# Optimization experiments

Measured on AMD Instinct MI355X. Metric: run time of the kernel, lower is better.

Reference implementation:

```python
import jax, jax.numpy as jnp
import numpy as np

# ---- module configuration (from init_kwargs) ----
NX, NV = 2048, 1024
LX = 1.0
VMAX = 6.0
DX = LX / NX
DV = 2.0 * VMAX / NV
XS = jnp.linspace(-LX / 2 + DX / 2, LX / 2 - DX / 2, NX)
VS = jnp.linspace(-VMAX + DV / 2, VMAX - DV / 2, NV)
AE, AI = 1.0, 1836.0
ZE, ZI = -1.0, 1.0
OMEGA_C_TAU = 1.0
NU_EE, NU_II = 1.0, 0.1
DT = 1e-3
T_LBO = 1.0  # LBO temperature, u = 0


def minmod(a, b):
    return jnp.where(a * b > 0, jnp.sign(a) * jnp.minimum(jnp.abs(a), jnp.abs(b)), 0.0)


def _sl(a, lo, hi, axis):
    return jax.lax.slice_in_dim(a, lo, hi, axis=axis)


def slope_limited_flux_divergence(f_pad, F, dx, axis):
    # f_pad has N+4 cells along `axis` (2 ghost cells per side). MUSCL + minmod.
    n = f_pad.shape[axis]
    d = _sl(f_pad, 1, n, axis) - _sl(f_pad, 0, n - 1, axis)          # n-1 diffs
    sigma = minmod(_sl(d, 0, n - 2, axis), _sl(d, 1, n - 1, axis))    # slopes for cells 1..n-2
    fc = _sl(f_pad, 1, n - 1, axis)                                   # cells 1..n-2
    m = n - 2
    fL = _sl(fc, 0, m - 1, axis) + 0.5 * _sl(sigma, 0, m - 1, axis)   # left interface states
    fR = _sl(fc, 1, m, axis) - 0.5 * _sl(sigma, 1, m, axis)           # right interface states
    flux = F(fL, fR)                                                  # N+1 interface fluxes
    k = flux.shape[axis]
    return (_sl(flux, 1, k, axis) - _sl(flux, 0, k - 1, axis)) / dx   # N cells


def pad_x_periodic(f):
    return jnp.concatenate([f[-2:, :], f, f[:2, :]], axis=0)


def pad_v_zero(f):
    z = jnp.zeros((f.shape[0], 2), f.dtype)
    return jnp.concatenate([z, f, z], axis=1)


def poisson_solve(rho_c):
    # dE/dx = rho_c, zero-mean E (periodic-compatible gauge)
    E = jnp.cumsum(rho_c) * DX
    return E - jnp.mean(E)


def species_rhs(f, E, A, Z):
    v = VS[None, :]
    Fx = lambda l, r: jnp.where(v > 0, l * v, r * v)                  # upwind in x
    vdfdx = slope_limited_flux_divergence(pad_x_periodic(f), Fx, DX, axis=0)
    Ec = (OMEGA_C_TAU * Z / A) * E[:, None]
    Fv = lambda l, r: jnp.where(Ec > 0, l * Ec, r * Ec)               # upwind in v
    Edfdv = slope_limited_flux_divergence(pad_v_zero(f), Fv, DV, axis=1)
    return -vdfdx - Edfdv


def vlasov_rhs(fe, fi):
    ne = jnp.sum(fe, axis=1) * DV
    ni = jnp.sum(fi, axis=1) * DV
    E = poisson_solve(ZE * ne + ZI * ni)
    return species_rhs(fe, E, AE, ZE), species_rhs(fi, E, AI, ZI)


def ssprk2(fe, fi, dt):
    re, ri = vlasov_rhs(fe, fi)
    fe1, fi1 = fe + dt * re, fi + dt * ri
    re1, ri1 = vlasov_rhs(fe1, fi1)
    return 0.5 * (fe + fe1 + dt * re1), 0.5 * (fi + fi1 + dt * ri1)


def lbo_diagonals(lam):
    # L f = lam * d/dv( v f + T df/dv ), central differences
    vm = jnp.roll(VS, 1)
    vp = jnp.roll(VS, -1)
    dl = lam * (T_LBO / DV**2 - vm / (2 * DV))
    du = lam * (T_LBO / DV**2 + vp / (2 * DV))
    d = lam * (-2.0 * T_LBO / DV**2) * jnp.ones(NV, XS.dtype)
    return dl.at[0].set(0.0), d, du.at[-1].set(0.0)


def nu_shape():
    midpt = LX / 3
    ef = LX / 6 / 10
    h0 = lambda x: 1 + jnp.exp(x / ef - midpt / ef)
    return 1.0 / (0.5 * (h0(XS) + h0(-XS)))  # [Nx]


def thomas(dl, d, du, b):
    # Thomas algorithm; dl[0]==0 and du[-1]==0 assumed.
    def fwd(carry, inp):
        cp, bp = carry
        dli, di, dui, bi = inp
        m = di - dli * cp
        cpi = dui / m
        bpi = (bi - dli * bp) / m
        return (cpi, bpi), (cpi, bpi)
    z = jnp.zeros((), b.dtype)
    _, (cp, bp) = jax.lax.scan(fwd, (z, z), (dl, d, du, b))
    def bwd(x_next, inp):
        cpi, bpi = inp
        x = bpi - cpi * x_next
        return x, x
    _, x = jax.lax.scan(bwd, z, (cp, bp), reverse=True)
    return x


def implicit_collide(f, lam, dt):
    dl, d, du = lbo_diagonals(lam)
    nu = nu_shape()
    def solve_row(nui, frow):
        return thomas(-dt * nui * dl, 1.0 - dt * nui * d, -dt * nui * du, frow)
    return jax.vmap(solve_row)(nu, f)


def setup_inputs() -> dict:
    key = jax.random.key(0)
    k1, k2 = jax.random.split(key)
    fe = jax.random.uniform(k1, (NX, NV), dtype=jnp.float32)
    fi = jax.random.uniform(k2, (NX, NV), dtype=jnp.float32)
    return {"fe": fe, "fi": fi}


def reference(fe, fi):
    fe1, fi1 = ssprk2(fe, fi, DT)
    fe2 = implicit_collide(fe1, NU_EE, DT)
    fi2 = implicit_collide(fi1, NU_II, DT)
    return jnp.stack([fe2, fi2])  # [2, Nx, Nv]
```

## Files before the change

### kernel.cpp

```cpp
#include <hip/hip_runtime.h>
#include <math.h>

#define NX 2048
#define NV 1024
static constexpr float DXf   = 1.0f / 2048.0f;
static constexpr float DVf   = 12.0f / 1024.0f;
static constexpr float DTf   = 0.001f;
static constexpr float INV_DX = 2048.0f;
static constexpr float INV_DV = 1024.0f / 12.0f;

__device__ __forceinline__ float minmod_f(float a, float b) {
    return (a * b > 0.0f) ? (a > 0.0f ? fminf(a, b) : fmaxf(a, b)) : 0.0f;
}

__device__ __forceinline__ float frcp(float x) {
    float r = __builtin_amdgcn_rcpf(x);
    return r * (2.0f - x * r);
}

__device__ __forceinline__ void rhs4(const float* __restrict__ g, int i, int j0, float Ec,
                                     float4& f0v, float4& rv) {
    const float* rowc = g + i * NV;
    const float* rm1  = g + (((i - 1) & (NX - 1)) * NV);
    const float* rm2  = g + (((i - 2) & (NX - 1)) * NV);
    const float* rp1  = g + (((i + 1) & (NX - 1)) * NV);
    const float* rp2  = g + (((i + 2) & (NX - 1)) * NV);

    float4 c   = *(const float4*)(rowc + j0);
    float4 xm1 = *(const float4*)(rm1 + j0);
    float4 xm2 = *(const float4*)(rm2 + j0);
    float4 xp1 = *(const float4*)(rp1 + j0);
    float4 xp2 = *(const float4*)(rp2 + j0);
    float4 lm = make_float4(0.f, 0.f, 0.f, 0.f);
    float4 rp = make_float4(0.f, 0.f, 0.f, 0.f);
    if (j0 >= 4)      lm = *(const float4*)(rowc + j0 - 4);
    if (j0 <= NV - 8) rp = *(const float4*)(rowc + j0 + 4);

    float vals[8] = {lm.z, lm.w, c.x, c.y, c.z, c.w, rp.x, rp.y};
    const float* cc   = (const float*)&c;
    const float* am1  = (const float*)&xm1;
    const float* am2  = (const float*)&xm2;
    const float* ap1  = (const float*)&xp1;
    const float* ap2  = (const float*)&xp2;
    float* f0o = (float*)&f0v;
    float* ro  = (float*)&rv;

    #pragma unroll
    for (int k = 0; k < 4; ++k) {
        float f0  = cc[k];
        float fm1 = am1[k], fm2 = am2[k], fp1 = ap1[k], fp2 = ap2[k];

        float v = DVf * ((float)(j0 + k) + 0.5f) - 6.0f;
        float dm1 = fm1 - fm2, d0 = f0 - fm1, dp1 = fp1 - f0, dp2 = fp2 - fp1;
        float sm1 = minmod_f(dm1, d0);
        float s0  = minmod_f(d0, dp1);
        float sp1 = minmod_f(dp1, dp2);
        float PhiM, PhiP;
        if (v > 0.0f) {
            PhiM = (fm1 + 0.5f * sm1) * v;
            PhiP = (f0  + 0.5f * s0 ) * v;
        } else {
            PhiM = (f0  - 0.5f * s0 ) * v;
            PhiP = (fp1 - 0.5f * sp1) * v;
        }
        float vdfdx = (PhiP - PhiM) * INV_DX;

        float gm2 = vals[k], gm1 = vals[k + 1], gp1 = vals[k + 3], gp2 = vals[k + 4];
        float em1 = gm1 - gm2, e0 = f0 - gm1, ep1 = gp1 - f0, ep2 = gp2 - gp1;
        float tm1 = minmod_f(em1, e0);
        float t0  = minmod_f(e0, ep1);
        float tp1 = minmod_f(ep1, ep2);
        float GM, GP;
        if (Ec > 0.0f) {
            GM = (gm1 + 0.5f * tm1) * Ec;
            GP = (f0  + 0.5f * t0 ) * Ec;
        } else {
            GM = (f0  - 0.5f * t0 ) * Ec;
            GP = (gp1 - 0.5f * tp1) * Ec;
        }
        float Edfdv = (GP - GM) * INV_DV;

        f0o[k] = f0;
        ro[k]  = -vdfdx - Edfdv;
    }
}

__device__ __forceinline__ float compute_E(const float* __restrict__ se,
                                           const float* __restrict__ si, int i) {
    int t = threadIdx.x;
    float pref = 0.0f, wtot = 0.0f;
    #pragma unroll
    for (int q = 0; q < NX / 256; ++q) {
        int k = q * 256 + t;
        float rho = DVf * (si[k] - se[k]);
        if (k <= i) pref += rho;
        wtot += rho * (float)(NX - k);
    }
    #pragma unroll
    for (int off = 32; off > 0; off >>= 1) {
        pref += __shfl_down(pref, off, 64);
        wtot += __shfl_down(wtot, off, 64);
    }
    __shared__ float sp[4], sw[4];
    int lane = t & 63, wave = t >> 6;
    if (lane == 0) { sp[wave] = pref; sw[wave] = wtot; }
    __syncthreads();
    float P = sp[0] + sp[1] + sp[2] + sp[3];
    float W = sw[0] + sw[1] + sw[2] + sw[3];
    return DXf * (P - W * (1.0f / (float)NX));
}

__global__ __launch_bounds__(256) void moments_kernel(const float* __restrict__ fe,
                                                      const float* __restrict__ fi,
                                                      float* __restrict__ se,
                                                      float* __restrict__ si) {
    int i = blockIdx.x;
    int t = threadIdx.x;
    float4 a4 = *(const float4*)(fe + (size_t)i * NV + 4 * t);
    float4 b4 = *(const float4*)(fi + (size_t)i * NV + 4 * t);
    float a = a4.x + a4.y + a4.z + a4.w;
    float b = b4.x + b4.y + b4.z + b4.w;
    __shared__ float r1[4], r2[4];
    #pragma unroll
    for (int off = 32; off > 0; off >>= 1) {
        a += __shfl_down(a, off, 64);
        b += __shfl_down(b, off, 64);
    }
    int lane = t & 63, wave = t >> 6;
    if (lane == 0) { r1[wave] = a; r2[wave] = b; }
    __syncthreads();
    if (t == 0) {
        se[i] = r1[0] + r1[1] + r1[2] + r1[3];
        si[i] = r2[0] + r2[1] + r2[2] + r2[3];
    }
}

__global__ __launch_bounds__(256) void stage1_kernel(const float* __restrict__ fe,
                                                     const float* __restrict__ fi,
                                                     const float* __restrict__ se,
                                                     const float* __restrict__ si,
                                                     float* __restrict__ fe1,
                                                     float* __restrict__ fi1,
                                                     float* __restrict__ se1,
                                                     float* __restrict__ si1) {
    int i  = blockIdx.x;
    int sp = blockIdx.y;
    const float* g = sp ? fi : fe;
    float* out = sp ? fi1 : fe1;
    float zoa = sp ? (1.0f / 1836.0f) : -1.0f;
    float Ec = zoa * compute_E(se, si, i);
    int t = threadIdx.x;
    int j0 = 4 * t;

    float4 f0v, rv;
    rhs4(g, i, j0, Ec, f0v, rv);
    float4 o;
    o.x = f0v.x + DTf * rv.x;
    o.y = f0v.y + DTf * rv.y;
    o.z = f0v.z + DTf * rv.z;
    o.w = f0v.w + DTf * rv.w;
    *(float4*)(out + i * NV + j0) = o;

    float x = o.x + o.y + o.z + o.w;
    #pragma unroll
    for (int off = 32; off > 0; off >>= 1) x += __shfl_down(x, off, 64);
    __shared__ float sred[4];
    int lane = t & 63, wave = t >> 6;
    if (lane == 0) sred[wave] = x;
    __syncthreads();
    if (t == 0) { (sp ? si1 : se1)[i] = sred[0] + sred[1] + sred[2] + sred[3]; }
}

__global__ __launch_bounds__(256) void stage2_collide_kernel(const float* __restrict__ fe,
                                                             const float* __restrict__ fi,
                                                             const float* __restrict__ fe1,
                                                             const float* __restrict__ fi1,
                                                             const float* __restrict__ se1,
                                                             const float* __restrict__ si1,
                                                             float* __restrict__ out) {
    const float Tdv2   = 1.0f / (DVf * DVf);
    const float inv2dv = 0.5f / DVf;

    int i  = blockIdx.x;
    int sp = blockIdx.y;
    const float* h = sp ? fi : fe;
    const float* g = sp ? fi1 : fe1;
    float* orow = out + ((size_t)sp * NX + i) * NV;
    float zoa = sp ? (1.0f / 1836.0f) : -1.0f;
    float lam = sp ? 0.1f : 1.0f;
    float Ec = zoa * compute_E(se1, si1, i);
    int t = threadIdx.x;
    int lane = t & 63;
    int wave = t >> 6;

    __shared__ float lds_f[NV + NV / 16];

    {
        int j0 = 4 * t;
        float4 f0v, rv;
        rhs4(g, i, j0, Ec, f0v, rv);
        float4 h4 = *(const float4*)(h + i * NV + j0);
        int a = j0 + (j0 >> 4);
        lds_f[a]     = 0.5f * h4.x + 0.5f * f0v.x + (0.5f * DTf) * rv.x;
        lds_f[a + 1] = 0.5f * h4.y + 0.5f * f0v.y + (0.5f * DTf) * rv.y;
        lds_f[a + 2] = 0.5f * h4.z + 0.5f * f0v.z + (0.5f * DTf) * rv.z;
        lds_f[a + 3] = 0.5f * h4.w + 0.5f * f0v.w + (0.5f * DTf) * rv.w;
    }
    __syncthreads();
    if (wave != 0) return;

    float xi = DXf * ((float)i + 0.5f) - 0.5f;
    float nu = 1.0f / (1.0f + 0.5f * (expf(60.0f * xi - 20.0f) + expf(-60.0f * xi - 20.0f)));
    float K = DTf * nu * lam;
    float b = 1.0f + 2.0f * K * Tdv2;

    float Dv[16], Av[16], Cv[16];
    int j0 = lane * 16;
    int base = 17 * lane;
    #pragma unroll
    for (int r = 0; r < 16; ++r) {
        int j = j0 + r;
        float d = lds_f[base + r];
        float a = (j == 0)      ? 0.0f : -K * (Tdv2 - (DVf * ((float)j - 0.5f) - 6.0f) * inv2dv);
        float c = (j == NV - 1) ? 0.0f : -K * (Tdv2 + (DVf * ((float)j + 1.5f) - 6.0f) * inv2dv);
        if (r == 0) {
            float e = frcp(b);
            Dv[0] = e * d;
            Av[0] = e * a;
            Cv[0] = e * c;
        } else {
            float e = frcp(b - a * Cv[r - 1]);
            Dv[r] = e * (d - a * Dv[r - 1]);
            Av[r] = -e * a * Av[r - 1];
            Cv[r] = e * c;
        }
    }
    #pragma unroll
    for (int r = 14; r >= 0; --r) {
        Dv[r] = Dv[r] - Cv[r] * Dv[r + 1];
        Av[r] = Av[r] - Cv[r] * Av[r + 1];
        Cv[r] = -Cv[r] * Cv[r + 1];
    }

    float la = Av[0],  ra = Cv[0],  d0 = Dv[0];
    float lb = Av[15], rb = Cv[15], d1 = Dv[15];

    #pragma unroll
    for (int s = 1; s < 64; s <<= 1) {
        float lb_m = __shfl_up(lb, s, 64);
        float rb_m = __shfl_up(rb, s, 64);
        float d1_m = __shfl_up(d1, s, 64);
        if (lane < s) { lb_m = 0.0f; rb_m = 0.0f; d1_m = 0.0f; }
        float la_p = __shfl_down(la, s, 64);
        float ra_p = __shfl_down(ra, s, 64);
        float d0_p = __shfl_down(d0, s, 64);
        if (lane + s > 63) { la_p = 0.0f; ra_p = 0.0f; d0_p = 0.0f; }

        float m00 = 1.0f - la * rb_m;
        float m01 = -ra * la_p;
        float m10 = -lb * rb_m;
        float m11 = 1.0f - rb * la_p;
        float idet = frcp(m00 * m11 - m01 * m10);

        float Lr0 = -la * lb_m, Lr1 = -lb * lb_m;
        float Rr0 = -ra * ra_p, Rr1 = -rb * ra_p;
        float e0 = d0 - la * d1_m - ra * d0_p;
        float e1 = d1 - lb * d1_m - rb * d0_p;

        la = idet * (m11 * Lr0 - m01 * Lr1);
        lb = idet * (m00 * Lr1 - m10 * Lr0);
        ra = idet * (m11 * Rr0 - m01 * Rr1);
        rb = idet * (m00 * Rr1 - m10 * Rr0);
        d0 = idet * (m11 * e0 - m01 * e1);
        d1 = idet * (m00 * e1 - m10 * e0);
    }
    float zl = __shfl_up(d1, 1, 64);
    if (lane == 0) zl = 0.0f;
    float yr = __shfl_down(d0, 1, 64);
    if (lane == 63) yr = 0.0f;

    float x[16];
    #pragma unroll
    for (int r = 0; r < 16; ++r) x[r] = Dv[r] - Av[r] * zl - Cv[r] * yr;
    #pragma unroll
    for (int q = 0; q < 4; ++q) {
        float4 o;
        o.x = x[4 * q];
        o.y = x[4 * q + 1];
        o.z = x[4 * q + 2];
        o.w = x[4 * q + 3];
        *(float4*)(orow + j0 + 4 * q) = o;
    }
}

extern "C" void kernel_launch(void* const* d_in, const int* in_sizes, int n_in,
                              void* d_out, int out_size, void* d_ws, size_t ws_size,
                              hipStream_t stream) {
    const float* fe = (const float*)d_in[0];
    const float* fi = (const float*)d_in[1];
    float* out = (float*)d_out;
    const size_t P = (size_t)NX * NV;

    float* fe1 = (float*)d_ws;
    float* fi1 = fe1 + P;
    float* se  = fi1 + P;
    float* si  = se + NX;
    float* se1 = si + NX;
    float* si1 = se1 + NX;

    dim3 rgrid(NX, 2);

    moments_kernel<<<NX, 256, 0, stream>>>(fe, fi, se, si);
    stage1_kernel<<<rgrid, 256, 0, stream>>>(fe, fi, se, si, fe1, fi1, se1, si1);
    stage2_collide_kernel<<<rgrid, 256, 0, stream>>>(fe, fi, fe1, fi1, se1, si1, out);
}
```

Baseline: 112.9 us.

## Fuse three kernels into one cooperative persistent kernel with grid syncs

Replaces the three separate launches (moments, stage 1, stage 2 plus collide) with a single cooperative kernel of 1024 blocks that loops over row pairs and uses grid.sync between phases. The aim is to remove launch gaps and tail effects between kernels. In stage 2 each block handles two rows for both species, with each of its four waves doing one tridiagonal solve instead of one wave per block. If the cooperative launch fails, it falls back to the old three-kernel path. The risks are grid-sync overhead, lower occupancy from the larger LDS buffer, and the requirement that all 1024 blocks be co-resident.

```diff
diff --git a/kernel.cpp b/kernel.cpp
--- a/kernel.cpp
+++ b/kernel.cpp
@@ -1,5 +1,8 @@
 #include <hip/hip_runtime.h>
+#include <hip/hip_cooperative_groups.h>
 #include <math.h>
+
+namespace cg = cooperative_groups;
 
 #define NX 2048
 #define NV 1024
@@ -101,13 +104,208 @@
         pref += __shfl_down(pref, off, 64);
         wtot += __shfl_down(wtot, off, 64);
     }
-    __shared__ float sp[4], sw[4];
+    __shared__ float sp_[4], sw_[4];
     int lane = t & 63, wave = t >> 6;
-    if (lane == 0) { sp[wave] = pref; sw[wave] = wtot; }
+    if (lane == 0) { sp_[wave] = pref; sw_[wave] = wtot; }
     __syncthreads();
-    float P = sp[0] + sp[1] + sp[2] + sp[3];
-    float W = sw[0] + sw[1] + sw[2] + sw[3];
+    float P = sp_[0] + sp_[1] + sp_[2] + sp_[3];
+    float W = sw_[0] + sw_[1] + sw_[2] + sw_[3];
+    __syncthreads();
     return DXf * (P - W * (1.0f / (float)NX));
+}
+
+__device__ __forceinline__ void wave_solve_row(const float* __restrict__ ldsrow,
+                                               int i, float lam, float* __restrict__ orow) {
+    const float Tdv2   = 1.0f / (DVf * DVf);
+    const float inv2dv = 0.5f / DVf;
+    int lane = threadIdx.x & 63;
+
+    float xi = DXf * ((float)i + 0.5f) - 0.5f;
+    float nu = 1.0f / (1.0f + 0.5f * (expf(60.0f * xi - 20.0f) + expf(-60.0f * xi - 20.0f)));
+    float K = DTf * nu * lam;
+    float b = 1.0f + 2.0f * K * Tdv2;
+
+    float Dv[16], Av[16], Cv[16];
+    int j0 = lane * 16;
+    int base = 17 * lane;
+    #pragma unroll
+    for (int r = 0; r < 16; ++r) {
+        int j = j0 + r;
+        float d = ldsrow[base + r];
+        float a = (j == 0)      ? 0.0f : -K * (Tdv2 - (DVf * ((float)j - 0.5f) - 6.0f) * inv2dv);
+        float c = (j == NV - 1) ? 0.0f : -K * (Tdv2 + (DVf * ((float)j + 1.5f) - 6.0f) * inv2dv);
+        if (r == 0) {
+            float e = frcp(b);
+            Dv[0] = e * d;
+            Av[0] = e * a;
+            Cv[0] = e * c;
+        } else {
+            float e = frcp(b - a * Cv[r - 1]);
+            Dv[r] = e * (d - a * Dv[r - 1]);
+            Av[r] = -e * a * Av[r - 1];
+            Cv[r] = e * c;
+        }
+    }
+    #pragma unroll
+    for (int r = 14; r >= 0; --r) {
+        Dv[r] = Dv[r] - Cv[r] * Dv[r + 1];
+        Av[r] = Av[r] - Cv[r] * Av[r + 1];
+        Cv[r] = -Cv[r] * Cv[r + 1];
+    }
+
+    float la = Av[0],  ra = Cv[0],  d0 = Dv[0];
+    float lb = Av[15], rb = Cv[15], d1 = Dv[15];
+
+    #pragma unroll
+    for (int s = 1; s < 64; s <<= 1) {
+        float lb_m = __shfl_up(lb, s, 64);
+        float rb_m = __shfl_up(rb, s, 64);
+        float d1_m = __shfl_up(d1, s, 64);
+        if (lane < s) { lb_m = 0.0f; rb_m = 0.0f; d1_m = 0.0f; }
+        float la_p = __shfl_down(la, s, 64);
+        float ra_p = __shfl_down(ra, s, 64);
+        float d0_p = __shfl_down(d0, s, 64);
+        if (lane + s > 63) { la_p = 0.0f; ra_p = 0.0f; d0_p = 0.0f; }
+
+        float m00 = 1.0f - la * rb_m;
+        float m01 = -ra * la_p;
+        float m10 = -lb * rb_m;
+        float m11 = 1.0f - rb * la_p;
+        float idet = frcp(m00 * m11 - m01 * m10);
+
+        float Lr0 = -la * lb_m, Lr1 = -lb * lb_m;
+        float Rr0 = -ra * ra_p, Rr1 = -rb * ra_p;
+        float e0 = d0 - la * d1_m - ra * d0_p;
+        float e1 = d1 - lb * d1_m - rb * d0_p;
+
+        la = idet * (m11 * Lr0 - m01 * Lr1);
+        lb = idet * (m00 * Lr1 - m10 * Lr0);
+        ra = idet * (m11 * Rr0 - m01 * Rr1);
+        rb = idet * (m00 * Rr1 - m10 * Rr0);
+        d0 = idet * (m11 * e0 - m01 * e1);
+        d1 = idet * (m00 * e1 - m10 * e0);
+    }
+    float zl = __shfl_up(d1, 1, 64);
+    if (lane == 0) zl = 0.0f;
+    float yr = __shfl_down(d0, 1, 64);
+    if (lane == 63) yr = 0.0f;
+
+    float x[16];
+    #pragma unroll
+    for (int r = 0; r < 16; ++r) x[r] = Dv[r] - Av[r] * zl - Cv[r] * yr;
+    #pragma unroll
+    for (int q = 0; q < 4; ++q) {
+        float4 o;
+        o.x = x[4 * q];
+        o.y = x[4 * q + 1];
+        o.z = x[4 * q + 2];
+        o.w = x[4 * q + 3];
+        *(float4*)(orow + j0 + 4 * q) = o;
+    }
+}
+
+__global__ __launch_bounds__(256, 4) void fused_kernel(const float* __restrict__ fe,
+                                                       const float* __restrict__ fi,
+                                                       float* __restrict__ fe1,
+                                                       float* __restrict__ fi1,
+                                                       float* __restrict__ se,
+                                                       float* __restrict__ si,
+                                                       float* __restrict__ se1,
+                                                       float* __restrict__ si1,
+                                                       float* __restrict__ out) {
+    cg::grid_group grid = cg::this_grid();
+    int t = threadIdx.x;
+    int lane = t & 63, wave = t >> 6;
+
+    __shared__ float r1[4], r2[4];
+    __shared__ float lds_f[4][NV + NV / 16];
+
+    for (int i = blockIdx.x * 2; i < NX; i += gridDim.x * 2) {
+        #pragma unroll
+        for (int q = 0; q < 2; ++q) {
+            int row = i + q;
+            float4 a4 = *(const float4*)(fe + (size_t)row * NV + 4 * t);
+            float4 b4 = *(const float4*)(fi + (size_t)row * NV + 4 * t);
+            float a = a4.x + a4.y + a4.z + a4.w;
+            float bb = b4.x + b4.y + b4.z + b4.w;
+            #pragma unroll
+            for (int off = 32; off > 0; off >>= 1) {
+                a  += __shfl_down(a, off, 64);
+                bb += __shfl_down(bb, off, 64);
+            }
+            if (lane == 0) { r1[wave] = a; r2[wave] = bb; }
+            __syncthreads();
+            if (t == 0) {
+                se[row] = r1[0] + r1[1] + r1[2] + r1[3];
+                si[row] = r2[0] + r2[1] + r2[2] + r2[3];
+            }
+            __syncthreads();
+        }
+    }
+    grid.sync();
+
+    for (int i2 = blockIdx.x * 2; i2 < NX; i2 += gridDim.x * 2) {
+        float E0 = compute_E(se, si, i2);
+        float E1 = compute_E(se, si, i2 + 1);
+        #pragma unroll
+        for (int k = 0; k < 4; ++k) {
+            int i  = i2 + (k >> 1);
+            int sp = k & 1;
+            float Ec = (sp ? (1.0f / 1836.0f) : -1.0f) * ((k >> 1) ? E1 : E0);
+            const float* g = sp ? fi : fe;
+            float* o = sp ? fi1 : fe1;
+            int j0 = 4 * t;
+            float4 f0v, rv;
+            rhs4(g, i, j0, Ec, f0v, rv);
+            float4 ov;
+            ov.x = f0v.x + DTf * rv.x;
+            ov.y = f0v.y + DTf * rv.y;
+            ov.z = f0v.z + DTf * rv.z;
+            ov.w = f0v.w + DTf * rv.w;
+            *(float4*)(o + i * NV + j0) = ov;
+
+            float x = ov.x + ov.y + ov.z + ov.w;
+            #pragma unroll
+            for (int off = 32; off > 0; off >>= 1) x += __shfl_down(x, off, 64);
+            if (lane == 0) r1[wave] = x;
+            __syncthreads();
+            if (t == 0) (sp ? si1 : se1)[i] = r1[0] + r1[1] + r1[2] + r1[3];
+            __syncthreads();
+        }
+    }
+    grid.sync();
+
+    for (int i2 = blockIdx.x * 2; i2 < NX; i2 += gridDim.x * 2) {
+        float F0 = compute_E(se1, si1, i2);
+        float F1 = compute_E(se1, si1, i2 + 1);
+        #pragma unroll
+        for (int k = 0; k < 4; ++k) {
+            int i  = i2 + (k >> 1);
+            int sp = k & 1;
+            float Ec = (sp ? (1.0f / 1836.0f) : -1.0f) * ((k >> 1) ? F1 : F0);
+            const float* g = sp ? fi1 : fe1;
+            const float* h = sp ? fi : fe;
+            int j0 = 4 * t;
+            float4 f0v, rv;
+            rhs4(g, i, j0, Ec, f0v, rv);
+            float4 h4 = *(const float4*)(h + i * NV + j0);
+            int a = j0 + (j0 >> 4);
+            lds_f[k][a]     = 0.5f * h4.x + 0.5f * f0v.x + (0.5f * DTf) * rv.x;
+            lds_f[k][a + 1] = 0.5f * h4.y + 0.5f * f0v.y + (0.5f * DTf) * rv.y;
+            lds_f[k][a + 2] = 0.5f * h4.z + 0.5f * f0v.z + (0.5f * DTf) * rv.z;
+            lds_f[k][a + 3] = 0.5f * h4.w + 0.5f * f0v.w + (0.5f * DTf) * rv.w;
+        }
+        __syncthreads();
+        {
+            int k  = wave;
+            int i  = i2 + (k >> 1);
+            int sp = k & 1;
+            float lam = sp ? 0.1f : 1.0f;
+            float* orow = out + ((size_t)sp * NX + i) * NV;
+            wave_solve_row(lds_f[k], i, lam, orow);
+        }
+        __syncthreads();
+    }
 }
 
 __global__ __launch_bounds__(256) void moments_kernel(const float* __restrict__ fe,
@@ -178,9 +376,6 @@
                                                              const float* __restrict__ se1,
                                                              const float* __restrict__ si1,
                                                              float* __restrict__ out) {
-    const float Tdv2   = 1.0f / (DVf * DVf);
-    const float inv2dv = 0.5f / DVf;
-
     int i  = blockIdx.x;
     int sp = blockIdx.y;
     const float* h = sp ? fi : fe;
@@ -190,11 +385,9 @@
     float lam = sp ? 0.1f : 1.0f;
     float Ec = zoa * compute_E(se1, si1, i);
     int t = threadIdx.x;
-    int lane = t & 63;
     int wave = t >> 6;
 
     __shared__ float lds_f[NV + NV / 16];
-
     {
         int j0 = 4 * t;
         float4 f0v, rv;
@@ -208,89 +401,7 @@
     }
     __syncthreads();
     if (wave != 0) return;
-
-    float xi = DXf * ((float)i + 0.5f) - 0.5f;
-    float nu = 1.0f / (1.0f + 0.5f * (expf(60.0f * xi - 20.0f) + expf(-60.0f * xi - 20.0f)));
-    float K = DTf * nu * lam;
-    float b = 1.0f + 2.0f * K * Tdv2;
-
-    float Dv[16], Av[16], Cv[16];
-    int j0 = lane * 16;
-    int base = 17 * lane;
-    #pragma unroll
-    for (int r = 0; r < 16; ++r) {
-        int j = j0 + r;
-        float d = lds_f[base + r];
-        float a = (j == 0)      ? 0.0f : -K * (Tdv2 - (DVf * ((float)j - 0.5f) - 6.0f) * inv2dv);
-        float c = (j == NV - 1) ? 0.0f : -K * (Tdv2 + (DVf * ((float)j + 1.5f) - 6.0f) * inv2dv);
-        if (r == 0) {
-            float e = frcp(b);
-            Dv[0] = e * d;
-            Av[0] = e * a;
-            Cv[0] = e * c;
-        } else {
-            float e = frcp(b - a * Cv[r - 1]);
-            Dv[r] = e * (d - a * Dv[r - 1]);
-            Av[r] = -e * a * Av[r - 1];
-            Cv[r] = e * c;
-        }
-    }
-    #pragma unroll
-    for (int r = 14; r >= 0; --r) {
-        Dv[r] = Dv[r] - Cv[r] * Dv[r + 1];
-        Av[r] = Av[r] - Cv[r] * Av[r + 1];
-        Cv[r] = -Cv[r] * Cv[r + 1];
-    }
-
-    float la = Av[0],  ra = Cv[0],  d0 = Dv[0];
-    float lb = Av[15], rb = Cv[15], d1 = Dv[15];
-
-    #pragma unroll
-    for (int s = 1; s < 64; s <<= 1) {
-        float lb_m = __shfl_up(lb, s, 64);
-        float rb_m = __shfl_up(rb, s, 64);
-        float d1_m = __shfl_up(d1, s, 64);
-        if (lane < s) { lb_m = 0.0f; rb_m = 0.0f; d1_m = 0.0f; }
-        float la_p = __shfl_down(la, s, 64);
-        float ra_p = __shfl_down(ra, s, 64);
-        float d0_p = __shfl_down(d0, s, 64);
-        if (lane + s > 63) { la_p = 0.0f; ra_p = 0.0f; d0_p = 0.0f; }
-
-        float m00 = 1.0f - la * rb_m;
-        float m01 = -ra * la_p;
-        float m10 = -lb * rb_m;
-        float m11 = 1.0f - rb * la_p;
-        float idet = frcp(m00 * m11 - m01 * m10);
-
-        float Lr0 = -la * lb_m, Lr1 = -lb * lb_m;
-        float Rr0 = -ra * ra_p, Rr1 = -rb * ra_p;
-        float e0 = d0 - la * d1_m - ra * d0_p;
-        float e1 = d1 - lb * d1_m - rb * d0_p;
-
-        la = idet * (m11 * Lr0 - m01 * Lr1);
-        lb = idet * (m00 * Lr1 - m10 * Lr0);
-        ra = idet * (m11 * Rr0 - m01 * Rr1);
-        rb = idet * (m00 * Rr1 - m10 * Rr0);
-        d0 = idet * (m11 * e0 - m01 * e1);
-        d1 = idet * (m00 * e1 - m10 * e0);
-    }
-    float zl = __shfl_up(d1, 1, 64);
-    if (lane == 0) zl = 0.0f;
-    float yr = __shfl_down(d0, 1, 64);
-    if (lane == 63) yr = 0.0f;
-
-    float x[16];
-    #pragma unroll
-    for (int r = 0; r < 16; ++r) x[r] = Dv[r] - Av[r] * zl - Cv[r] * yr;
-    #pragma unroll
-    for (int q = 0; q < 4; ++q) {
-        float4 o;
-        o.x = x[4 * q];
-        o.y = x[4 * q + 1];
-        o.z = x[4 * q + 2];
-        o.w = x[4 * q + 3];
-        *(float4*)(orow + j0 + 4 * q) = o;
-    }
+    wave_solve_row(lds_f, i, lam, orow);
 }
 
 extern "C" void kernel_launch(void* const* d_in, const int* in_sizes, int n_in,
@@ -308,9 +419,15 @@
     float* se1 = si + NX;
     float* si1 = se1 + NX;
 
-    dim3 rgrid(NX, 2);
-
-    moments_kernel<<<NX, 256, 0, stream>>>(fe, fi, se, si);
-    stage1_kernel<<<rgrid, 256, 0, stream>>>(fe, fi, se, si, fe1, fi1, se1, si1);
-    stage2_collide_kernel<<<rgrid, 256, 0, stream>>>(fe, fi, fe1, fi1, se1, si1, out);
-}
+    void* args[] = {(void*)&fe, (void*)&fi, (void*)&fe1, (void*)&fi1,
+                    (void*)&se, (void*)&si, (void*)&se1, (void*)&si1, (void*)&out};
+    hipError_t err = hipLaunchCooperativeKernel((const void*)fused_kernel,
+                                                dim3(1024), dim3(256),
+                                                args, 0, stream);
+    if (err != hipSuccess) {
+        dim3 rgrid(NX, 2);
+        moments_kernel<<<NX, 256, 0, stream>>>(fe, fi, se, si);
+        stage1_kernel<<<rgrid, 256, 0, stream>>>(fe, fi, se, si, fe1, fi1, se1, si1);
+        stage2_collide_kernel<<<rgrid, 256, 0, stream>>>(fe, fi, fe1, fi1, se1, si1, out);
+    }
+}
```

Result: slower. 313.1 us (+177.2%).
